# Optimization experiments

Measured on AMD Instinct MI355X. Metric: run time of the kernel, lower is better.

Reference implementation:

```python
import jax, jax.numpy as jnp
import numpy as np
from itertools import combinations

Nt, Nrf, Nk, FEAT, BATCH = 64, 4, 8, 512, 1024
Ng = Nt // Nk                      # 8
_MAX = len(list(combinations(range(Ng), Nrf)))  # 70
CSETSIZE = int(2 ** np.floor(np.log2(_MAX)))    # 64
SQRT_NRF = np.float32(np.sqrt(Nrf))


def _generate_antenna_selection_set(num_target):
    """Max-hamming-distance antenna selection set (numpy, matches torch code)."""
    combs = list(combinations(range(Ng), Nrf))
    maxSize = len(combs)
    globalSet = np.zeros((maxSize, Nt, Nrf), np.float32)
    for i, act in enumerate(combs):
        for j, a in enumerate(act):
            globalSet[i, a * Nk:a * Nk + Nk, j] = 1.0
    gsum = globalSet.sum(-1)  # (maxSize, Nt)
    selectSet = np.zeros((num_target, Nt, Nrf), np.float32)
    available = []
    for idx in range(num_target):
        if len(available) == 0:
            available = list(range(maxSize))
        if idx == 0:
            hd = np.zeros(len(available))
        else:
            sel = selectSet[:idx].sum(-1)            # (idx, Nt)
            cand = gsum[np.array(available)]          # (nAvail, Nt)
            hd = (sel[None, :, :] != cand[:, None, :]).sum(axis=(1, 2))
        sid = available[int(np.argmax(hd))]
        selectSet[idx] = globalSet[sid]
        available.remove(sid)
    return selectSet


def setup_inputs() -> dict:
    key = jax.random.key(0)
    ks = jax.random.split(key, 7)
    s = 1.0 / np.sqrt(FEAT)
    DDIM = CSETSIZE * Nrf * Nrf
    return {
        "x": jax.random.normal(ks[0], (BATCH, FEAT), jnp.float32),
        "W_A": jax.random.normal(ks[1], (Nt, FEAT), jnp.float32) * s,
        "b_A": jax.random.normal(ks[2], (Nt,), jnp.float32) * s,
        "W_Dr": jax.random.normal(ks[3], (DDIM, FEAT), jnp.float32) * s,
        "b_Dr": jax.random.normal(ks[4], (DDIM,), jnp.float32) * s,
        "W_Di": jax.random.normal(ks[5], (DDIM, FEAT), jnp.float32) * s,
        "b_Di": jax.random.normal(ks[6], (DDIM,), jnp.float32) * s,
        "CSet": jnp.asarray(_generate_antenna_selection_set(CSETSIZE)),
    }


def reference(x, W_A, b_A, W_Dr, b_Dr, W_Di, b_Di, CSet):
    B = x.shape[0]
    theta = x @ W_A.T + b_A                          # (B, Nt)
    cosT, sinT = jnp.cos(theta), jnp.sin(theta)
    eye = jnp.eye(Nt, dtype=x.dtype)
    A_real = (cosT[:, :, None] * eye)[:, None]       # (B, 1, Nt, Nt) diag-embed
    A_imag = (sinT[:, :, None] * eye)[:, None]
    D_real = (x @ W_Dr.T + b_Dr).reshape(B, CSETSIZE, Nrf, Nrf)
    D_imag = (x @ W_Di.T + b_Di).reshape(B, CSETSIZE, Nrf, Nrf)
    # diag(cos) @ C == row-scale of C (identical math to the dense matmul)
    ArC = cosT[:, None, :, None] * CSet[None]        # (B, CSetSize, Nt, Nrf)
    AiC = sinT[:, None, :, None] * CSet[None]
    ArCDr = ArC @ D_real
    ArCDi = ArC @ D_imag
    AiCDr = AiC @ D_real
    AiCDi = AiC @ D_imag
    V_real = ArCDr - AiCDi                           # (B, CSetSize, Nt, Nrf)
    V_imag = ArCDi + AiCDr
    V_F = jnp.sqrt(jnp.sum(V_real ** 2 + V_imag ** 2, axis=(2, 3)))
    V_F = V_F[:, :, None, None]
    D_real_n = SQRT_NRF * D_real / V_F
    D_imag_n = SQRT_NRF * D_imag / V_F
    return (A_real, A_imag, D_real_n, D_imag_n, CSet)
```

## Files before the change

### kernel.cpp

```cpp
#include <hip/hip_runtime.h>
#include <math.h>

#define BATCH 1024
#define FEAT  512
#define NT    64
#define DDIM  1024
#define BKA   32
#define LDSS  68


__global__ __launch_bounds__(256) void fused_kernel(
    const float* __restrict__ x,
    const float* __restrict__ W_A,  const float* __restrict__ b_A,
    const float* __restrict__ W_Dr, const float* __restrict__ b_Dr,
    const float* __restrict__ W_Di, const float* __restrict__ b_Di,
    const float* __restrict__ cset,
    float* __restrict__ out)
{
    const int bid = blockIdx.x;
    const int tid = threadIdx.x;

    if (bid < 256) {
        __shared__ __align__(16) float As [BKA][LDSS];
        __shared__ __align__(16) float Brs[BKA][LDSS];
        __shared__ __align__(16) float Bis[BKA][LDSS];

        const int bx = bid & 15;
        const int by = bid >> 4;
        const int row0 = by * 64;
        const int woff = bx * 64;

        const int srow = tid >> 2;
        const int skq  = (tid * 2) & 7;
        const float* xg  = x    + (size_t)(row0 + srow) * FEAT + skq * 4;
        const float* wrg = W_Dr + (size_t)(woff + srow) * FEAT + skq * 4;
        const float* wig = W_Di + (size_t)(woff + srow) * FEAT + skq * 4;

        const int r0 = (tid & 15) * 4;
        const int c0 = (tid >> 4) * 4;

        float accr[4][4] = {};
        float acci[4][4] = {};

        for (int k0 = 0; k0 < FEAT; k0 += BKA) {
            const float4 av0 = *(const float4*)(xg  + k0);
            const float4 av1 = *(const float4*)(xg  + k0 + 4);
            const float4 br0 = *(const float4*)(wrg + k0);
            const float4 br1 = *(const float4*)(wrg + k0 + 4);
            const float4 bi0 = *(const float4*)(wig + k0);
            const float4 bi1 = *(const float4*)(wig + k0 + 4);
            __syncthreads();
            const int kb = skq * 4;
            As [kb+0][srow]=av0.x; As [kb+1][srow]=av0.y; As [kb+2][srow]=av0.z; As [kb+3][srow]=av0.w;
            As [kb+4][srow]=av1.x; As [kb+5][srow]=av1.y; As [kb+6][srow]=av1.z; As [kb+7][srow]=av1.w;
            Brs[kb+0][srow]=br0.x; Brs[kb+1][srow]=br0.y; Brs[kb+2][srow]=br0.z; Brs[kb+3][srow]=br0.w;
            Brs[kb+4][srow]=br1.x; Brs[kb+5][srow]=br1.y; Brs[kb+6][srow]=br1.z; Brs[kb+7][srow]=br1.w;
            Bis[kb+0][srow]=bi0.x; Bis[kb+1][srow]=bi0.y; Bis[kb+2][srow]=bi0.z; Bis[kb+3][srow]=bi0.w;
            Bis[kb+4][srow]=bi1.x; Bis[kb+5][srow]=bi1.y; Bis[kb+6][srow]=bi1.z; Bis[kb+7][srow]=bi1.w;
            __syncthreads();

            #pragma unroll
            for (int k = 0; k < BKA; ++k) {
                const float4 a4  = *(const float4*)&As [k][r0];
                const float4 br4 = *(const float4*)&Brs[k][c0];
                const float4 bi4 = *(const float4*)&Bis[k][c0];
                const float a[4]  = {a4.x, a4.y, a4.z, a4.w};
                const float br[4] = {br4.x, br4.y, br4.z, br4.w};
                const float bi[4] = {bi4.x, bi4.y, bi4.z, bi4.w};
                #pragma unroll
                for (int i = 0; i < 4; ++i) {
                    #pragma unroll
                    for (int j = 0; j < 4; ++j) {
                        accr[i][j] += a[i] * br[j];
                        acci[i][j] += a[i] * bi[j];
                    }
                }
            }
        }

        const float4 bsr = *(const float4*)(b_Dr + woff + c0);
        const float4 bsi = *(const float4*)(b_Di + woff + c0);
        const float brv[4] = {bsr.x, bsr.y, bsr.z, bsr.w};
        const float biv[4] = {bsi.x, bsi.y, bsi.z, bsi.w};
        #pragma unroll
        for (int i = 0; i < 4; ++i)
            #pragma unroll
            for (int j = 0; j < 4; ++j) {
                accr[i][j] += brv[j];
                acci[i][j] += biv[j];
            }

        const size_t drn = (size_t)2 * BATCH * 4096;
        const size_t din = drn + (size_t)BATCH * DDIM;
        #pragma unroll
        for (int i = 0; i < 4; ++i) {
            float p = 0.f;
            #pragma unroll
            for (int j = 0; j < 4; ++j)
                p += accr[i][j] * accr[i][j] + acci[i][j] * acci[i][j];
            p += __shfl_xor(p, 16);
            p += __shfl_xor(p, 32);
            const float scale = 2.0f / sqrtf(8.0f * p);
            float4 orr, oii;
            orr.x = accr[i][0]*scale; orr.y = accr[i][1]*scale;
            orr.z = accr[i][2]*scale; orr.w = accr[i][3]*scale;
            oii.x = acci[i][0]*scale; oii.y = acci[i][1]*scale;
            oii.z = acci[i][2]*scale; oii.w = acci[i][3]*scale;
            const size_t off = (size_t)(row0 + r0 + i) * DDIM + woff + c0;
            *(float4*)(out + drn + off) = orr;
            *(float4*)(out + din + off) = oii;
        }
    } else {
        __shared__ float cosT[NT], sinT[NT];
        const int b = bid - 256;
        const int t = tid >> 2;
        const int q = tid & 3;

        const float* xr = x   + (size_t)b * FEAT + q * 128;
        const float* wr = W_A + (size_t)t * FEAT + q * 128;
        float sum = 0.f;
        #pragma unroll 8
        for (int i = 0; i < 128; i += 4) {
            const float4 xv = *(const float4*)(xr + i);
            const float4 wv = *(const float4*)(wr + i);
            sum += xv.x*wv.x + xv.y*wv.y + xv.z*wv.z + xv.w*wv.w;
        }
        sum += __shfl_xor(sum, 1);
        sum += __shfl_xor(sum, 2);
        if (q == 0) {
            const float theta = sum + b_A[t];
            float s, c;
            sincosf(theta, &s, &c);
            cosT[t] = c; sinT[t] = s;
        }
        __syncthreads();

        float* ar = out + (size_t)b * 4096;
        float* ai = out + (size_t)BATCH * 4096 + (size_t)b * 4096;
        #pragma unroll
        for (int it = 0; it < 4; ++it) {
            const int idx = tid + it * 256;
            const int tt = idx >> 4;
            const int j0 = (idx & 15) * 4;
            float4 vr = {0.f, 0.f, 0.f, 0.f};
            float4 vi = {0.f, 0.f, 0.f, 0.f};
            if (tt >= j0 && tt < j0 + 4) {
                ((float*)&vr)[tt - j0] = cosT[tt];
                ((float*)&vi)[tt - j0] = sinT[tt];
            }
            ((float4*)ar)[idx] = vr;
            ((float4*)ai)[idx] = vi;
        }

        if (b < 16) {
            const size_t base = (size_t)2 * BATCH * 4096 + (size_t)2 * BATCH * DDIM;
            ((float4*)(out + base))[b * 256 + tid] = ((const float4*)cset)[b * 256 + tid];
        }
    }
}

extern "C" void kernel_launch(void* const* d_in, const int* in_sizes, int n_in,
                              void* d_out, int out_size, void* d_ws, size_t ws_size,
                              hipStream_t stream) {
    const float* x    = (const float*)d_in[0];
    const float* W_A  = (const float*)d_in[1];
    const float* b_A  = (const float*)d_in[2];
    const float* W_Dr = (const float*)d_in[3];
    const float* b_Dr = (const float*)d_in[4];
    const float* W_Di = (const float*)d_in[5];
    const float* b_Di = (const float*)d_in[6];
    const float* CSet = (const float*)d_in[7];
    float* out = (float*)d_out;

    fused_kernel<<<1280, 256, 0, stream>>>(x, W_A, b_A, W_Dr, b_Dr, W_Di, b_Di,
                                           CSet, out);
}
```

Baseline: 127.4 us.

## Use bf16 MFMA for the D projection GEMM with smaller row tiles

Replaces the FP32 FMA outer-product GEMM for D_real/D_imag with bf16 MFMA 16x16x32 instructions. x and the weights are rounded to bf16 with RNE before being staged in LDS. Row tiles shrink from 64 to 32, which doubles the GEMM block count to 512. The per-row norm reduction moves to shuffles across 16 lanes, and stores become scalar. This trades FP32 accuracy for matrix-core throughput and risks bf16 precision error in the outputs.

```diff
diff --git a/kernel.cpp b/kernel.cpp
--- a/kernel.cpp
+++ b/kernel.cpp
@@ -5,9 +5,22 @@
 #define FEAT  512
 #define NT    64
 #define DDIM  1024
-#define BKA   32
-#define LDSS  68
 
+typedef __attribute__((ext_vector_type(8))) short  short8;
+typedef __attribute__((ext_vector_type(4))) float  floatx4;
+
+__device__ __forceinline__ unsigned short bf16rne(float f) {
+    unsigned int u = __float_as_uint(f);
+    return (unsigned short)((u + 0x7fffu + ((u >> 16) & 1u)) >> 16);
+}
+__device__ __forceinline__ short8 pack8(const float4 a, const float4 b) {
+    short8 r;
+    r[0] = (short)bf16rne(a.x); r[1] = (short)bf16rne(a.y);
+    r[2] = (short)bf16rne(a.z); r[3] = (short)bf16rne(a.w);
+    r[4] = (short)bf16rne(b.x); r[5] = (short)bf16rne(b.y);
+    r[6] = (short)bf16rne(b.z); r[7] = (short)bf16rne(b.w);
+    return r;
+}
 
 __global__ __launch_bounds__(256) void fused_kernel(
     const float* __restrict__ x,
@@ -20,99 +33,92 @@
     const int bid = blockIdx.x;
     const int tid = threadIdx.x;
 
-    if (bid < 256) {
-        __shared__ __align__(16) float As [BKA][LDSS];
-        __shared__ __align__(16) float Brs[BKA][LDSS];
-        __shared__ __align__(16) float Bis[BKA][LDSS];
+    if (bid < 512) {
+        __shared__ __align__(16) unsigned short As[32][32];
+        __shared__ __align__(16) unsigned short Bs[128][32];
 
-        const int bx = bid & 15;
-        const int by = bid >> 4;
-        const int row0 = by * 64;
+        const int bx   = bid & 15;
+        const int by   = bid >> 4;
+        const int row0 = by * 32;
         const int woff = bx * 64;
 
-        const int srow = tid >> 2;
-        const int skq  = (tid * 2) & 7;
-        const float* xg  = x    + (size_t)(row0 + srow) * FEAT + skq * 4;
-        const float* wrg = W_Dr + (size_t)(woff + srow) * FEAT + skq * 4;
-        const float* wig = W_Di + (size_t)(woff + srow) * FEAT + skq * 4;
+        const int nb = tid & 127;
+        const int g0 = tid >> 7;
+        const float* wsrc = (nb < 64)
+            ? (W_Dr + (size_t)(woff + nb) * FEAT)
+            : (W_Di + (size_t)(woff + nb - 64) * FEAT);
+        const int ldsN = ((nb & 63) >> 4) * 32 + ((nb < 64) ? 0 : 16) + (nb & 15);
 
-        const int r0 = (tid & 15) * 4;
-        const int c0 = (tid >> 4) * 4;
+        const float* xsrc = x + (size_t)(row0 + (tid >> 2)) * FEAT + (tid & 3) * 8;
 
-        float accr[4][4] = {};
-        float acci[4][4] = {};
+        const int lane    = tid & 63;
+        const int wv      = tid >> 6;
+        const int ln      = lane & 15;
+        const int quad    = lane >> 4;
+        const int rowbase = (wv & 1) * 16;
+        const int ctbase  = (wv >> 1) * 4;
 
-        for (int k0 = 0; k0 < FEAT; k0 += BKA) {
-            const float4 av0 = *(const float4*)(xg  + k0);
-            const float4 av1 = *(const float4*)(xg  + k0 + 4);
-            const float4 br0 = *(const float4*)(wrg + k0);
-            const float4 br1 = *(const float4*)(wrg + k0 + 4);
-            const float4 bi0 = *(const float4*)(wig + k0);
-            const float4 bi1 = *(const float4*)(wig + k0 + 4);
+        floatx4 acc[4] = {{0,0,0,0},{0,0,0,0},{0,0,0,0},{0,0,0,0}};
+
+        for (int k0 = 0; k0 < FEAT; k0 += 32) {
+            float4 xa0, xa1;
+            if (tid < 128) {
+                xa0 = *(const float4*)(xsrc + k0);
+                xa1 = *(const float4*)(xsrc + k0 + 4);
+            }
+            const float4 wa0 = *(const float4*)(wsrc + k0 + g0 * 8);
+            const float4 wa1 = *(const float4*)(wsrc + k0 + g0 * 8 + 4);
+            const float4 wb0 = *(const float4*)(wsrc + k0 + g0 * 8 + 16);
+            const float4 wb1 = *(const float4*)(wsrc + k0 + g0 * 8 + 20);
+
             __syncthreads();
-            const int kb = skq * 4;
-            As [kb+0][srow]=av0.x; As [kb+1][srow]=av0.y; As [kb+2][srow]=av0.z; As [kb+3][srow]=av0.w;
-            As [kb+4][srow]=av1.x; As [kb+5][srow]=av1.y; As [kb+6][srow]=av1.z; As [kb+7][srow]=av1.w;
-            Brs[kb+0][srow]=br0.x; Brs[kb+1][srow]=br0.y; Brs[kb+2][srow]=br0.z; Brs[kb+3][srow]=br0.w;
-            Brs[kb+4][srow]=br1.x; Brs[kb+5][srow]=br1.y; Brs[kb+6][srow]=br1.z; Brs[kb+7][srow]=br1.w;
-            Bis[kb+0][srow]=bi0.x; Bis[kb+1][srow]=bi0.y; Bis[kb+2][srow]=bi0.z; Bis[kb+3][srow]=bi0.w;
-            Bis[kb+4][srow]=bi1.x; Bis[kb+5][srow]=bi1.y; Bis[kb+6][srow]=bi1.z; Bis[kb+7][srow]=bi1.w;
+            if (tid < 128)
+                *(short8*)&As[tid >> 2][(tid & 3) * 8] = pack8(xa0, xa1);
+            *(short8*)&Bs[ldsN][g0 * 8]      = pack8(wa0, wa1);
+            *(short8*)&Bs[ldsN][g0 * 8 + 16] = pack8(wb0, wb1);
             __syncthreads();
 
+            const short8 a = *(const short8*)&As[rowbase + ln][quad * 8];
             #pragma unroll
-            for (int k = 0; k < BKA; ++k) {
-                const float4 a4  = *(const float4*)&As [k][r0];
-                const float4 br4 = *(const float4*)&Brs[k][c0];
-                const float4 bi4 = *(const float4*)&Bis[k][c0];
-                const float a[4]  = {a4.x, a4.y, a4.z, a4.w};
-                const float br[4] = {br4.x, br4.y, br4.z, br4.w};
-                const float bi[4] = {bi4.x, bi4.y, bi4.z, bi4.w};
-                #pragma unroll
-                for (int i = 0; i < 4; ++i) {
-                    #pragma unroll
-                    for (int j = 0; j < 4; ++j) {
-                        accr[i][j] += a[i] * br[j];
-                        acci[i][j] += a[i] * bi[j];
-                    }
-                }
+            for (int t = 0; t < 4; ++t) {
+                const short8 b = *(const short8*)&Bs[(ctbase + t) * 16 + ln][quad * 8];
+                acc[t] = __builtin_amdgcn_mfma_f32_16x16x32_bf16(a, b, acc[t], 0, 0, 0);
             }
         }
-
-        const float4 bsr = *(const float4*)(b_Dr + woff + c0);
-        const float4 bsi = *(const float4*)(b_Di + woff + c0);
-        const float brv[4] = {bsr.x, bsr.y, bsr.z, bsr.w};
-        const float biv[4] = {bsi.x, bsi.y, bsi.z, bsi.w};
-        #pragma unroll
-        for (int i = 0; i < 4; ++i)
-            #pragma unroll
-            for (int j = 0; j < 4; ++j) {
-                accr[i][j] += brv[j];
-                acci[i][j] += biv[j];
-            }
 
         const size_t drn = (size_t)2 * BATCH * 4096;
         const size_t din = drn + (size_t)BATCH * DDIM;
         #pragma unroll
-        for (int i = 0; i < 4; ++i) {
-            float p = 0.f;
+        for (int p = 0; p < 2; ++p) {
+            const int cbg = bx * 4 + (wv >> 1) * 2 + p;
+            const int col = cbg * 16 + ln;
+            const float br = b_Dr[col];
+            const float bi = b_Di[col];
+            float dr[4], di[4], ps[4];
             #pragma unroll
-            for (int j = 0; j < 4; ++j)
-                p += accr[i][j] * accr[i][j] + acci[i][j] * acci[i][j];
-            p += __shfl_xor(p, 16);
-            p += __shfl_xor(p, 32);
-            const float scale = 2.0f / sqrtf(8.0f * p);
-            float4 orr, oii;
-            orr.x = accr[i][0]*scale; orr.y = accr[i][1]*scale;
-            orr.z = accr[i][2]*scale; orr.w = accr[i][3]*scale;
-            oii.x = acci[i][0]*scale; oii.y = acci[i][1]*scale;
-            oii.z = acci[i][2]*scale; oii.w = acci[i][3]*scale;
-            const size_t off = (size_t)(row0 + r0 + i) * DDIM + woff + c0;
-            *(float4*)(out + drn + off) = orr;
-            *(float4*)(out + din + off) = oii;
+            for (int i = 0; i < 4; ++i) {
+                dr[i] = acc[2 * p][i] + br;
+                di[i] = acc[2 * p + 1][i] + bi;
+                ps[i] = dr[i] * dr[i] + di[i] * di[i];
+            }
+            #pragma unroll
+            for (int i = 0; i < 4; ++i) {
+                ps[i] += __shfl_xor(ps[i], 1);
+                ps[i] += __shfl_xor(ps[i], 2);
+                ps[i] += __shfl_xor(ps[i], 4);
+                ps[i] += __shfl_xor(ps[i], 8);
+            }
+            #pragma unroll
+            for (int i = 0; i < 4; ++i) {
+                const float scale = 2.0f / sqrtf(8.0f * ps[i]);
+                const size_t row_g = (size_t)(row0 + rowbase + quad * 4 + i);
+                out[drn + row_g * DDIM + col] = dr[i] * scale;
+                out[din + row_g * DDIM + col] = di[i] * scale;
+            }
         }
     } else {
         __shared__ float cosT[NT], sinT[NT];
-        const int b = bid - 256;
+        const int b = bid - 512;
         const int t = tid >> 2;
         const int q = tid & 3;
 
@@ -123,14 +129,13 @@
         for (int i = 0; i < 128; i += 4) {
             const float4 xv = *(const float4*)(xr + i);
             const float4 wv = *(const float4*)(wr + i);
-            sum += xv.x*wv.x + xv.y*wv.y + xv.z*wv.z + xv.w*wv.w;
+            sum += xv.x * wv.x + xv.y * wv.y + xv.z * wv.z + xv.w * wv.w;
         }
         sum += __shfl_xor(sum, 1);
         sum += __shfl_xor(sum, 2);
         if (q == 0) {
-            const float theta = sum + b_A[t];
             float s, c;
-            sincosf(theta, &s, &c);
+            sincosf(sum + b_A[t], &s, &c);
             cosT[t] = c; sinT[t] = s;
         }
         __syncthreads();
@@ -172,6 +177,6 @@
     const float* CSet = (const float*)d_in[7];
     float* out = (float*)d_out;
 
-    fused_kernel<<<1280, 256, 0, stream>>>(x, W_A, b_A, W_Dr, b_Dr, W_Di, b_Di,
+    fused_kernel<<<1536, 256, 0, stream>>>(x, W_A, b_A, W_Dr, b_Dr, W_Di, b_Di,
                                            CSet, out);
 }
```

Result: slower. 133.1 us (+4.4%).
